# Optimization experiments

Hardware: AMD Instinct MI355X
Metric: run time of the kernel (lower is better)

## Reference

```python
import jax, jax.numpy as jnp
import numpy as np

N_ATOMS = 204800
NUM_GRAPHS = 4096
NUM_STEMS = 81920   # 20 stems per graph
NUM_JBONDS = 40960  # 10 jbonds per graph
DIM = 128
NUM_OUT_PER_STEM = 105


def setup_inputs() -> dict:
    key = jax.random.key(0)
    ks = jax.random.split(key, 8)
    s = 1.0 / np.sqrt(DIM)
    return {
        "per_atom_out": jax.random.normal(ks[0], (N_ATOMS, DIM), jnp.float32),
        "scalar_outs": jax.random.normal(ks[1], (NUM_GRAPHS, 2), jnp.float32),
        "stem_atmidx": jax.random.randint(ks[2], (NUM_STEMS,), 0, N_ATOMS),
        "jbond_atmidx": jax.random.randint(ks[3], (NUM_JBONDS, 2), 0, N_ATOMS),
        "num_graphs": NUM_GRAPHS,
        "W1s": jax.random.normal(ks[4], (DIM, DIM), jnp.float32) * s,
        "b1s": jnp.zeros((DIM,), jnp.float32),
        "W2s": jax.random.normal(ks[5], (DIM, NUM_OUT_PER_STEM), jnp.float32) * s,
        "b2s": jnp.zeros((NUM_OUT_PER_STEM,), jnp.float32),
        "W1j": jax.random.normal(ks[6], (DIM, DIM), jnp.float32) * s,
        "b1j": jnp.zeros((DIM,), jnp.float32),
        "W2j": jax.random.normal(ks[7], (DIM, 1), jnp.float32) * s,
        "b2j": jnp.zeros((1,), jnp.float32),
    }


def _mlp(x, W1, b1, W2, b2):
    h = jax.nn.leaky_relu(x @ W1 + b1, negative_slope=0.01)
    return h @ W2 + b2


def reference(per_atom_out, scalar_outs, stem_atmidx, jbond_atmidx, num_graphs,
              W1s, b1s, W2s, b2s, W1j, b1j, W2j, b2j):
    # Gather per-stem atom features, run stem MLP: [num_stems, 105]
    stem_preds = _mlp(per_atom_out[stem_atmidx], W1s, b1s, W2s, b2s)
    # Gather both atoms of each jbond, run jbond MLP, mean over the 2 atoms
    jb = _mlp(per_atom_out[jbond_atmidx.reshape(-1)], W1j, b1j, W2j, b2j)  # [num_jbonds*2, 1]
    jbond_preds = jb.reshape(jbond_atmidx.shape).mean(axis=1)  # [num_jbonds]

    stop_logit = scalar_outs[:, 1:2]                       # [G, 1]
    break_logits = jbond_preds.reshape((num_graphs, -1))   # [G, jbonds_per_graph]
    add_logits = stem_preds.reshape((num_graphs, -1))      # [G, stems_per_graph*105]
    actor_logits = jnp.concatenate([stop_logit, break_logits, add_logits], axis=1)
    value = scalar_outs[:, :1]
    return (value, actor_logits)
```

## Files before the change

### kernel.cpp

```cpp
#include <hip/hip_runtime.h>

#define DIM 128
#define NGRAPH 4096
#define NSTEM 81920
#define NJROW 81920
#define NOUT 105
#define COLS 2111
#define SPG 20
#define ROWS 64
#define XPAD 136
#define TT 4
#define NBSB 320
#define NBJB 320

typedef __attribute__((ext_vector_type(8))) short bf16x8;
typedef __attribute__((ext_vector_type(4))) float f32x4;

__device__ __forceinline__ unsigned short f2bf(float f) {
    unsigned int u = __builtin_bit_cast(unsigned int, f);
    return (unsigned short)((u + 0x7fffu + ((u >> 16) & 1u)) >> 16);
}
__device__ __forceinline__ unsigned int cvtpk(float lo, float hi) {
    unsigned int r;
    asm("v_cvt_pk_bf16_f32 %0, %1, %2" : "=v"(r) : "v"(lo), "v"(hi));
    return r;
}
__device__ __forceinline__ float lrelu(float v) { return v > 0.f ? v : 0.01f * v; }

__device__ __forceinline__ void lgkm_barrier() {
    asm volatile("s_waitcnt lgkmcnt(0)" ::: "memory");
    __builtin_amdgcn_s_barrier();
}

__global__ __launch_bounds__(256) void prep_kernel(
    const float* __restrict__ W1s, const float* __restrict__ W2s,
    const float* __restrict__ W1j, const float* __restrict__ so,
    short* __restrict__ ws, float* __restrict__ out)
{
    int b = blockIdx.x;
    if (b < 24) {
        int mat = b >> 3, rg = b & 7;
        const float* W; short* dst; int NT, N;
        if (mat == 0)      { W = W1s; dst = ws;         NT = 8; N = 128; }
        else if (mat == 1) { W = W2s; dst = ws + 16384; NT = 7; N = 105; }
        else               { W = W1j; dst = ws + 30720; NT = 8; N = 128; }
        int Npad = NT * 16;
        int r2 = threadIdx.x >> 7;
        int n  = threadIdx.x & 127;
        #pragma unroll
        for (int rr = 0; rr < 16; rr += 2) {
            int k = rg * 16 + rr + r2;
            if (n < Npad) {
                float v = (n < N) ? W[k * N + n] : 0.f;
                int kt = k >> 5, i = k & 7, sub = (k >> 3) & 3;
                int lane = sub * 16 + (n & 15), nt = n >> 4;
                dst[((kt * NT + nt) * 64 + lane) * 8 + i] = (short)f2bf(v);
            }
        }
    } else {
        int g = (b - 24) * 256 + threadIdx.x;
        if (g < NGRAPH) {
            float2 v = *(const float2*)(so + 2 * g);
            out[g] = v.x;
            out[NGRAPH + g * COLS] = v.y;
        }
    }
}

__device__ __forceinline__ void issue_gather(const float* __restrict__ atom,
                                             const int (&a)[4], int ko, float4 (&g)[8])
{
    #pragma unroll
    for (int q = 0; q < 4; ++q) {
        g[2*q]   = *(const float4*)(atom + a[q] * DIM + ko);
        g[2*q+1] = *(const float4*)(atom + a[q] * DIM + ko + 4);
    }
}

__device__ __forceinline__ void stage_lds(short (*X)[XPAD], int rb, int ko,
                                          const float4 (&g)[8])
{
    #pragma unroll
    for (int q = 0; q < 4; ++q) {
        uint4 p;
        p.x = cvtpk(g[2*q].x,   g[2*q].y);
        p.y = cvtpk(g[2*q].z,   g[2*q].w);
        p.z = cvtpk(g[2*q+1].x, g[2*q+1].y);
        p.w = cvtpk(g[2*q+1].z, g[2*q+1].w);
        *(uint4*)&X[q * 16 + rb][ko] = p;
    }
}

__global__ __launch_bounds__(256, 2) void fused_mlp(
    const float* __restrict__ atom,
    const int* __restrict__ sidx, const int* __restrict__ jidx,
    const short* __restrict__ wsp,
    const float* __restrict__ b1s, const float* __restrict__ b2s,
    const float* __restrict__ b1j,
    const float* __restrict__ W2j, const float* __restrict__ b2j,
    float* __restrict__ out)
{
    __shared__ short Xbuf[2][ROWS][XPAD];
    __shared__ short Hbuf[ROWS][XPAD];
    __shared__ float red[4][ROWS];
    const int tid = threadIdx.x;
    const bool isStem = blockIdx.x < NBSB;
    const int pb = isStem ? blockIdx.x : blockIdx.x - NBSB;
    const int w = tid >> 6, l = tid & 63;
    const int lq = l >> 4, lc = l & 15;
    const int rb = tid >> 4, ko = (tid & 15) * 8;

    const int*   idx = isStem ? sidx : jidx;
    const short* W1p = isStem ? wsp : wsp + 30720;
    const float* b1  = isStem ? b1s : b1j;
    const int tbase = pb * TT * ROWS;

    int a[TT][4];
    #pragma unroll
    for (int t = 0; t < TT; ++t)
        #pragma unroll
        for (int q = 0; q < 4; ++q)
            a[t][q] = idx[tbase + t * ROWS + q * 16 + rb];

    float4 g[8];
    issue_gather(atom, a[0], ko, g);

    bf16x8 wf1[4][2];
    #pragma unroll
    for (int kt = 0; kt < 4; ++kt)
        #pragma unroll
        for (int j = 0; j < 2; ++j)
            wf1[kt][j] = *(const bf16x8*)(W1p + ((kt * 8 + w * 2 + j) * 64 + l) * 8);

    float4 bb1[2];
    #pragma unroll
    for (int j = 0; j < 2; ++j)
        bb1[j] = *(const float4*)(b1 + (w * 2 + j) * 16 + lq * 4);

    bf16x8 wf2[4][2];
    float bb2[2];
    float4 wvj[2];
    float bj = 0.f;
    if (isStem) {
        const short* W2p = wsp + 16384;
        #pragma unroll
        for (int kt = 0; kt < 4; ++kt)
            #pragma unroll
            for (int j = 0; j < 2; ++j) {
                int nt = w * 2 + j; if (nt > 6) nt = 6;
                wf2[kt][j] = *(const bf16x8*)(W2p + ((kt * 7 + nt) * 64 + l) * 8);
            }
        #pragma unroll
        for (int j = 0; j < 2; ++j) {
            int c = (w * 2 + j) * 16 + lc;
            bb2[j] = (c < NOUT) ? b2s[c] : 0.f;
        }
    } else {
        #pragma unroll
        for (int j = 0; j < 2; ++j)
            wvj[j] = *(const float4*)(W2j + (w * 2 + j) * 16 + lq * 4);
        bj = b2j[0];
    }

    stage_lds(Xbuf[0], rb, ko, g);
    lgkm_barrier();

    if (isStem) {
        #pragma unroll
        for (int t = 0; t < TT; ++t) {
            if (t + 1 < TT) issue_gather(atom, a[t + 1], ko, g);

            f32x4 acc[4][2];
            #pragma unroll
            for (int j = 0; j < 2; ++j)
                #pragma unroll
                for (int m = 0; m < 4; ++m)
                    acc[m][j] = (f32x4){bb1[j].x, bb1[j].y, bb1[j].z, bb1[j].w};
            #pragma unroll
            for (int kt = 0; kt < 4; ++kt) {
                bf16x8 A0 = *(const bf16x8*)&Xbuf[t & 1][lc]     [kt * 32 + lq * 8];
                bf16x8 A1 = *(const bf16x8*)&Xbuf[t & 1][16 + lc][kt * 32 + lq * 8];
                bf16x8 A2 = *(const bf16x8*)&Xbuf[t & 1][32 + lc][kt * 32 + lq * 8];
                bf16x8 A3 = *(const bf16x8*)&Xbuf[t & 1][48 + lc][kt * 32 + lq * 8];
                #pragma unroll
                for (int j = 0; j < 2; ++j) {
                    acc[0][j] = __builtin_amdgcn_mfma_f32_16x16x32_bf16(wf1[kt][j], A0, acc[0][j], 0, 0, 0);
                    acc[1][j] = __builtin_amdgcn_mfma_f32_16x16x32_bf16(wf1[kt][j], A1, acc[1][j], 0, 0, 0);
                    acc[2][j] = __builtin_amdgcn_mfma_f32_16x16x32_bf16(wf1[kt][j], A2, acc[2][j], 0, 0, 0);
                    acc[3][j] = __builtin_amdgcn_mfma_f32_16x16x32_bf16(wf1[kt][j], A3, acc[3][j], 0, 0, 0);
                }
            }

            #pragma unroll
            for (int m = 0; m < 4; ++m)
                #pragma unroll
                for (int j = 0; j < 2; ++j) {
                    float r0 = lrelu(acc[m][j][0]), r1 = lrelu(acc[m][j][1]);
                    float r2 = lrelu(acc[m][j][2]), r3 = lrelu(acc[m][j][3]);
                    uint2 hp;
                    hp.x = cvtpk(r0, r1);
                    hp.y = cvtpk(r2, r3);
                    *(uint2*)&Hbuf[m * 16 + lc][(w * 2 + j) * 16 + lq * 4] = hp;
                }
            lgkm_barrier();

            f32x4 acc2[4][2];
            #pragma unroll
            for (int j = 0; j < 2; ++j)
                #pragma unroll
                for (int m = 0; m < 4; ++m)
                    acc2[m][j] = (f32x4){bb2[j], bb2[j], bb2[j], bb2[j]};
            #pragma unroll
            for (int kt = 0; kt < 4; ++kt) {
                bf16x8 A0 = *(const bf16x8*)&Hbuf[lc]     [kt * 32 + lq * 8];
                bf16x8 A1 = *(const bf16x8*)&Hbuf[16 + lc][kt * 32 + lq * 8];
                bf16x8 A2 = *(const bf16x8*)&Hbuf[32 + lc][kt * 32 + lq * 8];
                bf16x8 A3 = *(const bf16x8*)&Hbuf[48 + lc][kt * 32 + lq * 8];
                #pragma unroll
                for (int j = 0; j < 2; ++j) {
                    acc2[0][j] = __builtin_amdgcn_mfma_f32_16x16x32_bf16(A0, wf2[kt][j], acc2[0][j], 0, 0, 0);
                    acc2[1][j] = __builtin_amdgcn_mfma_f32_16x16x32_bf16(A1, wf2[kt][j], acc2[1][j], 0, 0, 0);
                    acc2[2][j] = __builtin_amdgcn_mfma_f32_16x16x32_bf16(A2, wf2[kt][j], acc2[2][j], 0, 0, 0);
                    acc2[3][j] = __builtin_amdgcn_mfma_f32_16x16x32_bf16(A3, wf2[kt][j], acc2[3][j], 0, 0, 0);
                }
            }

            if (t + 1 < TT) stage_lds(Xbuf[(t + 1) & 1], rb, ko, g);

            const int baseS = tbase + t * ROWS;
            #pragma unroll
            for (int m = 0; m < 4; ++m)
                #pragma unroll
                for (int rg = 0; rg < 4; ++rg) {
                    int S = baseS + m * 16 + lq * 4 + rg;
                    int gph = S / SPG, sl = S - gph * SPG;
                    float* ob = out + NGRAPH + gph * COLS + 1 + 10 + sl * NOUT;
                    #pragma unroll
                    for (int j = 0; j < 2; ++j) {
                        int c = (w * 2 + j) * 16 + lc;
                        if (c < NOUT) ob[c] = acc2[m][j][rg];
                    }
                }
            lgkm_barrier();
        }
    } else {
        #pragma unroll
        for (int t = 0; t < TT; ++t) {
            if (t + 1 < TT) issue_gather(atom, a[t + 1], ko, g);

            f32x4 acc[4][2];
            #pragma unroll
            for (int j = 0; j < 2; ++j)
                #pragma unroll
                for (int m = 0; m < 4; ++m)
                    acc[m][j] = (f32x4){bb1[j].x, bb1[j].y, bb1[j].z, bb1[j].w};
            #pragma unroll
            for (int kt = 0; kt < 4; ++kt) {
                bf16x8 A0 = *(const bf16x8*)&Xbuf[t & 1][lc]     [kt * 32 + lq * 8];
                bf16x8 A1 = *(const bf16x8*)&Xbuf[t & 1][16 + lc][kt * 32 + lq * 8];
                bf16x8 A2 = *(const bf16x8*)&Xbuf[t & 1][32 + lc][kt * 32 + lq * 8];
                bf16x8 A3 = *(const bf16x8*)&Xbuf[t & 1][48 + lc][kt * 32 + lq * 8];
                #pragma unroll
                for (int j = 0; j < 2; ++j) {
                    acc[0][j] = __builtin_amdgcn_mfma_f32_16x16x32_bf16(wf1[kt][j], A0, acc[0][j], 0, 0, 0);
                    acc[1][j] = __builtin_amdgcn_mfma_f32_16x16x32_bf16(wf1[kt][j], A1, acc[1][j], 0, 0, 0);
                    acc[2][j] = __builtin_amdgcn_mfma_f32_16x16x32_bf16(wf1[kt][j], A2, acc[2][j], 0, 0, 0);
                    acc[3][j] = __builtin_amdgcn_mfma_f32_16x16x32_bf16(wf1[kt][j], A3, acc[3][j], 0, 0, 0);
                }
            }

            float pf[4];
            #pragma unroll
            for (int m = 0; m < 4; ++m) {
                float p = 0.f;
                #pragma unroll
                for (int j = 0; j < 2; ++j) {
                    p += lrelu(acc[m][j][0]) * wvj[j].x;
                    p += lrelu(acc[m][j][1]) * wvj[j].y;
                    p += lrelu(acc[m][j][2]) * wvj[j].z;
                    p += lrelu(acc[m][j][3]) * wvj[j].w;
                }
                pf[m] = p;
            }
            #pragma unroll
            for (int m = 0; m < 4; ++m) {
                pf[m] += __shfl_xor(pf[m], 16, 64);
                pf[m] += __shfl_xor(pf[m], 32, 64);
            }
            if (l < 16)
                #pragma unroll
                for (int m = 0; m < 4; ++m)
                    red[w][m * 16 + l] = pf[m];
            lgkm_barrier();

            if (tid < 32) {
                int r0 = tid * 2;
                float s0 = red[0][r0] + red[1][r0] + red[2][r0] + red[3][r0];
                float s1 = red[0][r0+1] + red[1][r0+1] + red[2][r0+1] + red[3][r0+1];
                float v = (s0 + s1) * 0.5f + bj;
                int B = (pb * TT + t) * 32 + tid;
                int gg = B / 10, c = B - gg * 10;
                out[NGRAPH + gg * COLS + 1 + c] = v;
            }
            if (t + 1 < TT) stage_lds(Xbuf[(t + 1) & 1], rb, ko, g);
            lgkm_barrier();
        }
    }
}

extern "C" void kernel_launch(void* const* d_in, const int* in_sizes, int n_in,
                              void* d_out, int out_size, void* d_ws, size_t ws_size,
                              hipStream_t stream) {
    const float* per_atom_out = (const float*)d_in[0];
    const float* scalar_outs  = (const float*)d_in[1];
    const int*   stem_atmidx  = (const int*)d_in[2];
    const int*   jbond_atmidx = (const int*)d_in[3];
    const float* W1s = (const float*)d_in[5];
    const float* b1s = (const float*)d_in[6];
    const float* W2s = (const float*)d_in[7];
    const float* b2s = (const float*)d_in[8];
    const float* W1j = (const float*)d_in[9];
    const float* b1j = (const float*)d_in[10];
    const float* W2j = (const float*)d_in[11];
    const float* b2j = (const float*)d_in[12];
    float* out = (float*)d_out;
    short* wsp = (short*)d_ws;

    hipLaunchKernelGGL(prep_kernel, dim3(40), dim3(256), 0, stream,
                       W1s, W2s, W1j, scalar_outs, wsp, out);
    hipLaunchKernelGGL(fused_mlp, dim3(NBSB + NBJB), dim3(256), 0, stream,
                       per_atom_out, stem_atmidx, jbond_atmidx, wsp,
                       b1s, b2s, b1j, W2j, b2j, out);
}
```

Baseline: 33.03 us.

## Fold weight prep into fused kernel and reuse X buffer for hidden activations

Removes the separate weight-packing kernel: each block now reads the fp32 weights directly and packs them into bf16 MFMA fragments in registers, and scalar outputs are written by extra blocks of the same launch. The hidden-activation buffer is dropped by writing H into the current X slot after a barrier, which shrinks LDS so the launch bound can rise to 3 blocks per CU. Output stores become nontemporal. The trade is redundant strided weight loads and conversion in every block, plus an extra barrier per tile.

```diff
diff --git a/kernel.cpp b/kernel.cpp
--- a/kernel.cpp
+++ b/kernel.cpp
@@ -12,14 +12,11 @@
 #define TT 4
 #define NBSB 320
 #define NBJB 320
+#define NSCB 16
 
 typedef __attribute__((ext_vector_type(8))) short bf16x8;
 typedef __attribute__((ext_vector_type(4))) float f32x4;
 
-__device__ __forceinline__ unsigned short f2bf(float f) {
-    unsigned int u = __builtin_bit_cast(unsigned int, f);
-    return (unsigned short)((u + 0x7fffu + ((u >> 16) & 1u)) >> 16);
-}
 __device__ __forceinline__ unsigned int cvtpk(float lo, float hi) {
     unsigned int r;
     asm("v_cvt_pk_bf16_f32 %0, %1, %2" : "=v"(r) : "v"(lo), "v"(hi));
@@ -30,41 +27,6 @@
 __device__ __forceinline__ void lgkm_barrier() {
     asm volatile("s_waitcnt lgkmcnt(0)" ::: "memory");
     __builtin_amdgcn_s_barrier();
-}
-
-__global__ __launch_bounds__(256) void prep_kernel(
-    const float* __restrict__ W1s, const float* __restrict__ W2s,
-    const float* __restrict__ W1j, const float* __restrict__ so,
-    short* __restrict__ ws, float* __restrict__ out)
-{
-    int b = blockIdx.x;
-    if (b < 24) {
-        int mat = b >> 3, rg = b & 7;
-        const float* W; short* dst; int NT, N;
-        if (mat == 0)      { W = W1s; dst = ws;         NT = 8; N = 128; }
-        else if (mat == 1) { W = W2s; dst = ws + 16384; NT = 7; N = 105; }
-        else               { W = W1j; dst = ws + 30720; NT = 8; N = 128; }
-        int Npad = NT * 16;
-        int r2 = threadIdx.x >> 7;
-        int n  = threadIdx.x & 127;
-        #pragma unroll
-        for (int rr = 0; rr < 16; rr += 2) {
-            int k = rg * 16 + rr + r2;
-            if (n < Npad) {
-                float v = (n < N) ? W[k * N + n] : 0.f;
-                int kt = k >> 5, i = k & 7, sub = (k >> 3) & 3;
-                int lane = sub * 16 + (n & 15), nt = n >> 4;
-                dst[((kt * NT + nt) * 64 + lane) * 8 + i] = (short)f2bf(v);
-            }
-        }
-    } else {
-        int g = (b - 24) * 256 + threadIdx.x;
-        if (g < NGRAPH) {
-            float2 v = *(const float2*)(so + 2 * g);
-            out[g] = v.x;
-            out[NGRAPH + g * COLS] = v.y;
-        }
-    }
 }
 
 __device__ __forceinline__ void issue_gather(const float* __restrict__ atom,
@@ -91,27 +53,48 @@
     }
 }
 
-__global__ __launch_bounds__(256, 2) void fused_mlp(
+__device__ __forceinline__ bf16x8 pack_frag(const float* __restrict__ W,
+                                            int kt, int lq, int stride, int col)
+{
+    float e[8];
+    #pragma unroll
+    for (int i = 0; i < 8; ++i)
+        e[i] = W[(kt * 32 + lq * 8 + i) * stride + col];
+    uint4 p;
+    p.x = cvtpk(e[0], e[1]); p.y = cvtpk(e[2], e[3]);
+    p.z = cvtpk(e[4], e[5]); p.w = cvtpk(e[6], e[7]);
+    return __builtin_bit_cast(bf16x8, p);
+}
+
+__global__ __launch_bounds__(256, 3) void fused_all(
     const float* __restrict__ atom,
     const int* __restrict__ sidx, const int* __restrict__ jidx,
-    const short* __restrict__ wsp,
-    const float* __restrict__ b1s, const float* __restrict__ b2s,
-    const float* __restrict__ b1j,
+    const float* __restrict__ W1s, const float* __restrict__ b1s,
+    const float* __restrict__ W2s, const float* __restrict__ b2s,
+    const float* __restrict__ W1j, const float* __restrict__ b1j,
     const float* __restrict__ W2j, const float* __restrict__ b2j,
-    float* __restrict__ out)
+    const float* __restrict__ so, float* __restrict__ out)
 {
     __shared__ short Xbuf[2][ROWS][XPAD];
-    __shared__ short Hbuf[ROWS][XPAD];
     __shared__ float red[4][ROWS];
+    const int bid = blockIdx.x;
     const int tid = threadIdx.x;
-    const bool isStem = blockIdx.x < NBSB;
-    const int pb = isStem ? blockIdx.x : blockIdx.x - NBSB;
+
+    if (bid >= NBSB + NBJB) {
+        int gph = (bid - NBSB - NBJB) * 256 + tid;
+        float2 v = *(const float2*)(so + 2 * gph);
+        __builtin_nontemporal_store(v.x, &out[gph]);
+        __builtin_nontemporal_store(v.y, &out[NGRAPH + gph * COLS]);
+        return;
+    }
+
+    const bool isStem = bid < NBSB;
+    const int pb = isStem ? bid : bid - NBSB;
     const int w = tid >> 6, l = tid & 63;
     const int lq = l >> 4, lc = l & 15;
     const int rb = tid >> 4, ko = (tid & 15) * 8;
 
     const int*   idx = isStem ? sidx : jidx;
-    const short* W1p = isStem ? wsp : wsp + 30720;
     const float* b1  = isStem ? b1s : b1j;
     const int tbase = pb * TT * ROWS;
 
@@ -125,12 +108,13 @@
     float4 g[8];
     issue_gather(atom, a[0], ko, g);
 
+    const float* Wsrc1 = isStem ? W1s : W1j;
     bf16x8 wf1[4][2];
     #pragma unroll
     for (int kt = 0; kt < 4; ++kt)
         #pragma unroll
         for (int j = 0; j < 2; ++j)
-            wf1[kt][j] = *(const bf16x8*)(W1p + ((kt * 8 + w * 2 + j) * 64 + l) * 8);
+            wf1[kt][j] = pack_frag(Wsrc1, kt, lq, DIM, (w * 2 + j) * 16 + lc);
 
     float4 bb1[2];
     #pragma unroll
@@ -142,13 +126,13 @@
     float4 wvj[2];
     float bj = 0.f;
     if (isStem) {
-        const short* W2p = wsp + 16384;
         #pragma unroll
         for (int kt = 0; kt < 4; ++kt)
             #pragma unroll
             for (int j = 0; j < 2; ++j) {
-                int nt = w * 2 + j; if (nt > 6) nt = 6;
-                wf2[kt][j] = *(const bf16x8*)(W2p + ((kt * 7 + nt) * 64 + l) * 8);
+                int c = (w * 2 + j) * 16 + lc;
+                int cl = c > 104 ? 104 : c;
+                wf2[kt][j] = pack_frag(W2s, kt, lq, NOUT, cl);
             }
         #pragma unroll
         for (int j = 0; j < 2; ++j) {
@@ -168,6 +152,8 @@
     if (isStem) {
         #pragma unroll
         for (int t = 0; t < TT; ++t) {
+            short (*XA)[XPAD] = Xbuf[t & 1];
+            short (*XB)[XPAD] = Xbuf[(t + 1) & 1];
             if (t + 1 < TT) issue_gather(atom, a[t + 1], ko, g);
 
             f32x4 acc[4][2];
@@ -178,10 +164,10 @@
                     acc[m][j] = (f32x4){bb1[j].x, bb1[j].y, bb1[j].z, bb1[j].w};
             #pragma unroll
             for (int kt = 0; kt < 4; ++kt) {
-                bf16x8 A0 = *(const bf16x8*)&Xbuf[t & 1][lc]     [kt * 32 + lq * 8];
-                bf16x8 A1 = *(const bf16x8*)&Xbuf[t & 1][16 + lc][kt * 32 + lq * 8];
-                bf16x8 A2 = *(const bf16x8*)&Xbuf[t & 1][32 + lc][kt * 32 + lq * 8];
-                bf16x8 A3 = *(const bf16x8*)&Xbuf[t & 1][48 + lc][kt * 32 + lq * 8];
+                bf16x8 A0 = *(const bf16x8*)&XA[lc]     [kt * 32 + lq * 8];
+                bf16x8 A1 = *(const bf16x8*)&XA[16 + lc][kt * 32 + lq * 8];
+                bf16x8 A2 = *(const bf16x8*)&XA[32 + lc][kt * 32 + lq * 8];
+                bf16x8 A3 = *(const bf16x8*)&XA[48 + lc][kt * 32 + lq * 8];
                 #pragma unroll
                 for (int j = 0; j < 2; ++j) {
                     acc[0][j] = __builtin_amdgcn_mfma_f32_16x16x32_bf16(wf1[kt][j], A0, acc[0][j], 0, 0, 0);
@@ -190,17 +176,16 @@
                     acc[3][j] = __builtin_amdgcn_mfma_f32_16x16x32_bf16(wf1[kt][j], A3, acc[3][j], 0, 0, 0);
                 }
             }
+            lgkm_barrier();
 
             #pragma unroll
             for (int m = 0; m < 4; ++m)
                 #pragma unroll
                 for (int j = 0; j < 2; ++j) {
-                    float r0 = lrelu(acc[m][j][0]), r1 = lrelu(acc[m][j][1]);
-                    float r2 = lrelu(acc[m][j][2]), r3 = lrelu(acc[m][j][3]);
                     uint2 hp;
-                    hp.x = cvtpk(r0, r1);
-                    hp.y = cvtpk(r2, r3);
-                    *(uint2*)&Hbuf[m * 16 + lc][(w * 2 + j) * 16 + lq * 4] = hp;
+                    hp.x = cvtpk(lrelu(acc[m][j][0]), lrelu(acc[m][j][1]));
+                    hp.y = cvtpk(lrelu(acc[m][j][2]), lrelu(acc[m][j][3]));
+                    *(uint2*)&XA[m * 16 + lc][(w * 2 + j) * 16 + lq * 4] = hp;
                 }
             lgkm_barrier();
 
@@ -212,10 +197,10 @@
                     acc2[m][j] = (f32x4){bb2[j], bb2[j], bb2[j], bb2[j]};
             #pragma unroll
             for (int kt = 0; kt < 4; ++kt) {
-                bf16x8 A0 = *(const bf16x8*)&Hbuf[lc]     [kt * 32 + lq * 8];
-                bf16x8 A1 = *(const bf16x8*)&Hbuf[16 + lc][kt * 32 + lq * 8];
-                bf16x8 A2 = *(const bf16x8*)&Hbuf[32 + lc][kt * 32 + lq * 8];
-                bf16x8 A3 = *(const bf16x8*)&Hbuf[48 + lc][kt * 32 + lq * 8];
+                bf16x8 A0 = *(const bf16x8*)&XA[lc]     [kt * 32 + lq * 8];
+                bf16x8 A1 = *(const bf16x8*)&XA[16 + lc][kt * 32 + lq * 8];
+                bf16x8 A2 = *(const bf16x8*)&XA[32 + lc][kt * 32 + lq * 8];
+                bf16x8 A3 = *(const bf16x8*)&XA[48 + lc][kt * 32 + lq * 8];
                 #pragma unroll
                 for (int j = 0; j < 2; ++j) {
                     acc2[0][j] = __builtin_amdgcn_mfma_f32_16x16x32_bf16(A0, wf2[kt][j], acc2[0][j], 0, 0, 0);
@@ -224,8 +209,6 @@
                     acc2[3][j] = __builtin_amdgcn_mfma_f32_16x16x32_bf16(A3, wf2[kt][j], acc2[3][j], 0, 0, 0);
                 }
             }
-
-            if (t + 1 < TT) stage_lds(Xbuf[(t + 1) & 1], rb, ko, g);
 
             const int baseS = tbase + t * ROWS;
             #pragma unroll
@@ -238,14 +221,18 @@
                     #pragma unroll
                     for (int j = 0; j < 2; ++j) {
                         int c = (w * 2 + j) * 16 + lc;
-                        if (c < NOUT) ob[c] = acc2[m][j][rg];
+                        if (c < NOUT) __builtin_nontemporal_store(acc2[m][j][rg], &ob[c]);
                     }
                 }
+
+            if (t + 1 < TT) stage_lds(XB, rb, ko, g);
             lgkm_barrier();
         }
     } else {
         #pragma unroll
         for (int t = 0; t < TT; ++t) {
+            short (*XA)[XPAD] = Xbuf[t & 1];
+            short (*XB)[XPAD] = Xbuf[(t + 1) & 1];
             if (t + 1 < TT) issue_gather(atom, a[t + 1], ko, g);
 
             f32x4 acc[4][2];
@@ -256,10 +243,10 @@
                     acc[m][j] = (f32x4){bb1[j].x, bb1[j].y, bb1[j].z, bb1[j].w};
             #pragma unroll
             for (int kt = 0; kt < 4; ++kt) {
-                bf16x8 A0 = *(const bf16x8*)&Xbuf[t & 1][lc]     [kt * 32 + lq * 8];
-                bf16x8 A1 = *(const bf16x8*)&Xbuf[t & 1][16 + lc][kt * 32 + lq * 8];
-                bf16x8 A2 = *(const bf16x8*)&Xbuf[t & 1][32 + lc][kt * 32 + lq * 8];
-                bf16x8 A3 = *(const bf16x8*)&Xbuf[t & 1][48 + lc][kt * 32 + lq * 8];
+                bf16x8 A0 = *(const bf16x8*)&XA[lc]     [kt * 32 + lq * 8];
+                bf16x8 A1 = *(const bf16x8*)&XA[16 + lc][kt * 32 + lq * 8];
+                bf16x8 A2 = *(const bf16x8*)&XA[32 + lc][kt * 32 + lq * 8];
+                bf16x8 A3 = *(const bf16x8*)&XA[48 + lc][kt * 32 + lq * 8];
                 #pragma unroll
                 for (int j = 0; j < 2; ++j) {
                     acc[0][j] = __builtin_amdgcn_mfma_f32_16x16x32_bf16(wf1[kt][j], A0, acc[0][j], 0, 0, 0);
@@ -300,9 +287,9 @@
                 float v = (s0 + s1) * 0.5f + bj;
                 int B = (pb * TT + t) * 32 + tid;
                 int gg = B / 10, c = B - gg * 10;
-                out[NGRAPH + gg * COLS + 1 + c] = v;
-            }
-            if (t + 1 < TT) stage_lds(Xbuf[(t + 1) & 1], rb, ko, g);
+                __builtin_nontemporal_store(v, &out[NGRAPH + gg * COLS + 1 + c]);
+            }
+            if (t + 1 < TT) stage_lds(XB, rb, ko, g);
             lgkm_barrier();
         }
     }
@@ -324,11 +311,9 @@
     const float* W2j = (const float*)d_in[11];
     const float* b2j = (const float*)d_in[12];
     float* out = (float*)d_out;
-    short* wsp = (short*)d_ws;
-
-    hipLaunchKernelGGL(prep_kernel, dim3(40), dim3(256), 0, stream,
-                       W1s, W2s, W1j, scalar_outs, wsp, out);
-    hipLaunchKernelGGL(fused_mlp, dim3(NBSB + NBJB), dim3(256), 0, stream,
-                       per_atom_out, stem_atmidx, jbond_atmidx, wsp,
-                       b1s, b2s, b1j, W2j, b2j, out);
-}
+
+    hipLaunchKernelGGL(fused_all, dim3(NBSB + NBJB + NSCB), dim3(256), 0, stream,
+                       per_atom_out, stem_atmidx, jbond_atmidx,
+                       W1s, b1s, W2s, b2s, W1j, b1j, W2j, b2j,
+                       scalar_outs, out);
+}
```

New measurement: 42.60 us. 29.0% more time.

## Cut registers and LDS to raise occupancy to four blocks per CU

Applied to the files above, without the earlier changes.

Raises the launch bound from 2 to 4 blocks per CU. To make room it drops the separate hidden-activation LDS buffer and writes the hidden layer into the current X buffer, which needs an extra barrier. The second-layer stem weights are now reloaded from global/L2 on every k-step instead of being held in registers, and gather indices are prefetched two tiles ahead rather than all up front. The aim is more waves in flight to hide gather latency, paid for with extra weight loads and an added barrier.

```diff
diff --git a/kernel.cpp b/kernel.cpp
--- a/kernel.cpp
+++ b/kernel.cpp
@@ -91,7 +91,7 @@
     }
 }
 
-__global__ __launch_bounds__(256, 2) void fused_mlp(
+__global__ __launch_bounds__(256, 4) void fused_mlp(
     const float* __restrict__ atom,
     const int* __restrict__ sidx, const int* __restrict__ jidx,
     const short* __restrict__ wsp,
@@ -101,7 +101,6 @@
     float* __restrict__ out)
 {
     __shared__ short Xbuf[2][ROWS][XPAD];
-    __shared__ short Hbuf[ROWS][XPAD];
     __shared__ float red[4][ROWS];
     const int tid = threadIdx.x;
     const bool isStem = blockIdx.x < NBSB;
@@ -117,7 +116,7 @@
 
     int a[TT][4];
     #pragma unroll
-    for (int t = 0; t < TT; ++t)
+    for (int t = 0; t < 2; ++t)
         #pragma unroll
         for (int q = 0; q < 4; ++q)
             a[t][q] = idx[tbase + t * ROWS + q * 16 + rb];
@@ -137,22 +136,16 @@
     for (int j = 0; j < 2; ++j)
         bb1[j] = *(const float4*)(b1 + (w * 2 + j) * 16 + lq * 4);
 
-    bf16x8 wf2[4][2];
     float bb2[2];
+    int nt2[2];
     float4 wvj[2];
     float bj = 0.f;
     if (isStem) {
-        const short* W2p = wsp + 16384;
-        #pragma unroll
-        for (int kt = 0; kt < 4; ++kt)
-            #pragma unroll
-            for (int j = 0; j < 2; ++j) {
-                int nt = w * 2 + j; if (nt > 6) nt = 6;
-                wf2[kt][j] = *(const bf16x8*)(W2p + ((kt * 7 + nt) * 64 + l) * 8);
-            }
         #pragma unroll
         for (int j = 0; j < 2; ++j) {
-            int c = (w * 2 + j) * 16 + lc;
+            int nt = w * 2 + j;
+            nt2[j] = nt > 6 ? 6 : nt;
+            int c = nt * 16 + lc;
             bb2[j] = (c < NOUT) ? b2s[c] : 0.f;
         }
     } else {
@@ -166,9 +159,16 @@
     lgkm_barrier();
 
     if (isStem) {
+        const short* W2p = wsp + 16384;
         #pragma unroll
         for (int t = 0; t < TT; ++t) {
+            short (*XA)[XPAD] = Xbuf[t & 1];
+            short (*XB)[XPAD] = Xbuf[(t + 1) & 1];
             if (t + 1 < TT) issue_gather(atom, a[t + 1], ko, g);
+            if (t + 2 < TT)
+                #pragma unroll
+                for (int q = 0; q < 4; ++q)
+                    a[t + 2][q] = idx[tbase + (t + 2) * ROWS + q * 16 + rb];
 
             f32x4 acc[4][2];
             #pragma unroll
@@ -178,10 +178,10 @@
                     acc[m][j] = (f32x4){bb1[j].x, bb1[j].y, bb1[j].z, bb1[j].w};
             #pragma unroll
             for (int kt = 0; kt < 4; ++kt) {
-                bf16x8 A0 = *(const bf16x8*)&Xbuf[t & 1][lc]     [kt * 32 + lq * 8];
-                bf16x8 A1 = *(const bf16x8*)&Xbuf[t & 1][16 + lc][kt * 32 + lq * 8];
-                bf16x8 A2 = *(const bf16x8*)&Xbuf[t & 1][32 + lc][kt * 32 + lq * 8];
-                bf16x8 A3 = *(const bf16x8*)&Xbuf[t & 1][48 + lc][kt * 32 + lq * 8];
+                bf16x8 A0 = *(const bf16x8*)&XA[lc]     [kt * 32 + lq * 8];
+                bf16x8 A1 = *(const bf16x8*)&XA[16 + lc][kt * 32 + lq * 8];
+                bf16x8 A2 = *(const bf16x8*)&XA[32 + lc][kt * 32 + lq * 8];
+                bf16x8 A3 = *(const bf16x8*)&XA[48 + lc][kt * 32 + lq * 8];
                 #pragma unroll
                 for (int j = 0; j < 2; ++j) {
                     acc[0][j] = __builtin_amdgcn_mfma_f32_16x16x32_bf16(wf1[kt][j], A0, acc[0][j], 0, 0, 0);
@@ -190,17 +190,16 @@
                     acc[3][j] = __builtin_amdgcn_mfma_f32_16x16x32_bf16(wf1[kt][j], A3, acc[3][j], 0, 0, 0);
                 }
             }
+            lgkm_barrier();
 
             #pragma unroll
             for (int m = 0; m < 4; ++m)
                 #pragma unroll
                 for (int j = 0; j < 2; ++j) {
-                    float r0 = lrelu(acc[m][j][0]), r1 = lrelu(acc[m][j][1]);
-                    float r2 = lrelu(acc[m][j][2]), r3 = lrelu(acc[m][j][3]);
                     uint2 hp;
-                    hp.x = cvtpk(r0, r1);
-                    hp.y = cvtpk(r2, r3);
-                    *(uint2*)&Hbuf[m * 16 + lc][(w * 2 + j) * 16 + lq * 4] = hp;
+                    hp.x = cvtpk(lrelu(acc[m][j][0]), lrelu(acc[m][j][1]));
+                    hp.y = cvtpk(lrelu(acc[m][j][2]), lrelu(acc[m][j][3]));
+                    *(uint2*)&XA[m * 16 + lc][(w * 2 + j) * 16 + lq * 4] = hp;
                 }
             lgkm_barrier();
 
@@ -212,20 +211,22 @@
                     acc2[m][j] = (f32x4){bb2[j], bb2[j], bb2[j], bb2[j]};
             #pragma unroll
             for (int kt = 0; kt < 4; ++kt) {
-                bf16x8 A0 = *(const bf16x8*)&Hbuf[lc]     [kt * 32 + lq * 8];
-                bf16x8 A1 = *(const bf16x8*)&Hbuf[16 + lc][kt * 32 + lq * 8];
-                bf16x8 A2 = *(const bf16x8*)&Hbuf[32 + lc][kt * 32 + lq * 8];
-                bf16x8 A3 = *(const bf16x8*)&Hbuf[48 + lc][kt * 32 + lq * 8];
-                #pragma unroll
-                for (int j = 0; j < 2; ++j) {
-                    acc2[0][j] = __builtin_amdgcn_mfma_f32_16x16x32_bf16(A0, wf2[kt][j], acc2[0][j], 0, 0, 0);
-                    acc2[1][j] = __builtin_amdgcn_mfma_f32_16x16x32_bf16(A1, wf2[kt][j], acc2[1][j], 0, 0, 0);
-                    acc2[2][j] = __builtin_amdgcn_mfma_f32_16x16x32_bf16(A2, wf2[kt][j], acc2[2][j], 0, 0, 0);
-                    acc2[3][j] = __builtin_amdgcn_mfma_f32_16x16x32_bf16(A3, wf2[kt][j], acc2[3][j], 0, 0, 0);
-                }
-            }
-
-            if (t + 1 < TT) stage_lds(Xbuf[(t + 1) & 1], rb, ko, g);
+                bf16x8 wf2[2];
+                #pragma unroll
+                for (int j = 0; j < 2; ++j)
+                    wf2[j] = *(const bf16x8*)(W2p + ((kt * 7 + nt2[j]) * 64 + l) * 8);
+                bf16x8 A0 = *(const bf16x8*)&XA[lc]     [kt * 32 + lq * 8];
+                bf16x8 A1 = *(const bf16x8*)&XA[16 + lc][kt * 32 + lq * 8];
+                bf16x8 A2 = *(const bf16x8*)&XA[32 + lc][kt * 32 + lq * 8];
+                bf16x8 A3 = *(const bf16x8*)&XA[48 + lc][kt * 32 + lq * 8];
+                #pragma unroll
+                for (int j = 0; j < 2; ++j) {
+                    acc2[0][j] = __builtin_amdgcn_mfma_f32_16x16x32_bf16(A0, wf2[j], acc2[0][j], 0, 0, 0);
+                    acc2[1][j] = __builtin_amdgcn_mfma_f32_16x16x32_bf16(A1, wf2[j], acc2[1][j], 0, 0, 0);
+                    acc2[2][j] = __builtin_amdgcn_mfma_f32_16x16x32_bf16(A2, wf2[j], acc2[2][j], 0, 0, 0);
+                    acc2[3][j] = __builtin_amdgcn_mfma_f32_16x16x32_bf16(A3, wf2[j], acc2[3][j], 0, 0, 0);
+                }
+            }
 
             const int baseS = tbase + t * ROWS;
             #pragma unroll
@@ -241,12 +242,20 @@
                         if (c < NOUT) ob[c] = acc2[m][j][rg];
                     }
                 }
+
+            if (t + 1 < TT) stage_lds(XB, rb, ko, g);
             lgkm_barrier();
         }
     } else {
         #pragma unroll
         for (int t = 0; t < TT; ++t) {
+            short (*XA)[XPAD] = Xbuf[t & 1];
+            short (*XB)[XPAD] = Xbuf[(t + 1) & 1];
             if (t + 1 < TT) issue_gather(atom, a[t + 1], ko, g);
+            if (t + 2 < TT)
+                #pragma unroll
+                for (int q = 0; q < 4; ++q)
+                    a[t + 2][q] = idx[tbase + (t + 2) * ROWS + q * 16 + rb];
 
             f32x4 acc[4][2];
             #pragma unroll
@@ -256,10 +265,10 @@
                     acc[m][j] = (f32x4){bb1[j].x, bb1[j].y, bb1[j].z, bb1[j].w};
             #pragma unroll
             for (int kt = 0; kt < 4; ++kt) {
-                bf16x8 A0 = *(const bf16x8*)&Xbuf[t & 1][lc]     [kt * 32 + lq * 8];
-                bf16x8 A1 = *(const bf16x8*)&Xbuf[t & 1][16 + lc][kt * 32 + lq * 8];
-                bf16x8 A2 = *(const bf16x8*)&Xbuf[t & 1][32 + lc][kt * 32 + lq * 8];
-                bf16x8 A3 = *(const bf16x8*)&Xbuf[t & 1][48 + lc][kt * 32 + lq * 8];
+                bf16x8 A0 = *(const bf16x8*)&XA[lc]     [kt * 32 + lq * 8];
+                bf16x8 A1 = *(const bf16x8*)&XA[16 + lc][kt * 32 + lq * 8];
+                bf16x8 A2 = *(const bf16x8*)&XA[32 + lc][kt * 32 + lq * 8];
+                bf16x8 A3 = *(const bf16x8*)&XA[48 + lc][kt * 32 + lq * 8];
                 #pragma unroll
                 for (int j = 0; j < 2; ++j) {
                     acc[0][j] = __builtin_amdgcn_mfma_f32_16x16x32_bf16(wf1[kt][j], A0, acc[0][j], 0, 0, 0);
@@ -302,7 +311,7 @@
                 int gg = B / 10, c = B - gg * 10;
                 out[NGRAPH + gg * COLS + 1 + c] = v;
             }
-            if (t + 1 < TT) stage_lds(Xbuf[(t + 1) & 1], rb, ko, g);
+            if (t + 1 < TT) stage_lds(XB, rb, ko, g);
             lgkm_barrier();
         }
     }
```

Result: slower. 62.13 us (+88.1%).
